# Optimization experiments

Measured on AMD Instinct MI355X. Metric: run time of the kernel, lower is better.

Reference implementation:

```python
import jax, jax.numpy as jnp
import numpy as np
import math

LENS = 64  # sliding window length (init arg `lens`)

def setup_inputs() -> dict:
    key = jax.random.key(0)
    k1, k2 = jax.random.split(key)
    N, D = 4096, 512
    X = jax.random.normal(k1, (N, D), dtype=jnp.float32)
    # nn.Linear(d, d, bias=False) weight, applied as x @ W.T
    W = jax.random.normal(k2, (D, D), dtype=jnp.float32) * (1.0 / math.sqrt(D))
    return {"X": X, "W": W}

def reference(X, W):
    N, d = X.shape
    B = N - LENS  # number of sliding windows
    # sliding-window gather: h_his[b] = X[b : b+LENS]
    idx = jnp.arange(B)[:, None] + jnp.arange(LENS)[None, :]  # [B, LENS]
    h_his = X[idx]            # [B, LENS, d]
    h_cur = X[LENS:]          # [B, d]  (index_cur = lens..N-1)
    # attention: score = bmm(linear(kv), q[..., None]) / sqrt(d)
    kv_proj = jnp.einsum('bld,ed->ble', h_his, W)            # [B, LENS, d]
    score = jnp.einsum('ble,be->bl', kv_proj, h_cur)[..., None] / math.sqrt(d)  # [B, LENS, 1]
    # faithful to original: softmax over last (size-1) axis -> all ones
    alpha = jax.nn.softmax(score, axis=-1)                   # [B, LENS, 1]
    attn_out = jnp.einsum('bl,bld->bd', alpha[..., 0], h_his)  # [B, d]
    # dropout(0.3) is eval-mode identity
    H = jnp.concatenate([X[:LENS], attn_out], axis=0) + X    # [N, d]
    h_cur_full = jnp.concatenate([X[:LENS], h_cur], axis=0)  # [N, d]
    return jnp.concatenate([H, h_cur_full], axis=-1)         # [N, 2d]
```

## Files before the change

kernel.cpp:

```cpp
#include <hip/hip_runtime.h>


#define LENS 64
#define RT 8
#define C4 128

__global__ __launch_bounds__(256) void chunk8_kernel(const float4* __restrict__ X4,
                                                     float4* __restrict__ C8,
                                                     int nChunks) {
    const int t  = blockIdx.x * 256 + threadIdx.x;
    const int c4 = t & (C4 - 1);
    const int k  = t >> 7;
    if (k >= nChunks) return;
    const float4* p = X4 + (size_t)k * 8 * C4 + c4;
    float4 s = make_float4(0.f, 0.f, 0.f, 0.f);
#pragma unroll
    for (int j = 0; j < 8; ++j) {
        float4 x = p[(size_t)j * C4];
        s.x += x.x; s.y += x.y; s.z += x.z; s.w += x.w;
    }
    C8[(size_t)k * C4 + c4] = s;
}

__global__ __launch_bounds__(256) void winsum_kernel(const float4* __restrict__ X4,
                                                     const float4* __restrict__ C8,
                                                     float4* __restrict__ O4,
                                                     int N) {
    const int c4   = threadIdx.x & (C4 - 1);
    const int half = threadIdx.x >> 7;
    const int i0   = blockIdx.x * (2 * RT) + half * RT;
    if (i0 >= N) return;

    if (i0 < LENS) {
#pragma unroll
        for (int k = 0; k < RT; ++k) {
            const int i = i0 + k;
            float4 x = X4[(size_t)i * C4 + c4];
            float4 h = make_float4(2.f * x.x, 2.f * x.y, 2.f * x.z, 2.f * x.w);
            O4[(size_t)i * (2 * C4) + c4]      = h;
            O4[(size_t)i * (2 * C4) + C4 + c4] = x;
        }
        return;
    }

    const int m = i0 >> 3;
    float4 w = make_float4(0.f, 0.f, 0.f, 0.f);
#pragma unroll
    for (int q = 0; q < 8; ++q) {
        float4 cs = C8[(size_t)(m - 8 + q) * C4 + c4];
        w.x += cs.x; w.y += cs.y; w.z += cs.z; w.w += cs.w;
    }

    float4 hist[RT - 1];
    const float4* ph = X4 + (size_t)(i0 - LENS) * C4 + c4;
#pragma unroll
    for (int j = 0; j < RT - 1; ++j) hist[j] = ph[(size_t)j * C4];

#pragma unroll
    for (int k = 0; k < RT; ++k) {
        const int i = i0 + k;
        float4 x = X4[(size_t)i * C4 + c4];
        float4 h = make_float4(x.x + w.x, x.y + w.y, x.z + w.z, x.w + w.w);
        O4[(size_t)i * (2 * C4) + c4]      = h;
        O4[(size_t)i * (2 * C4) + C4 + c4] = x;
        if (k < RT - 1) {
            float4 old = hist[k];
            w.x += x.x - old.x;
            w.y += x.y - old.y;
            w.z += x.z - old.z;
            w.w += x.w - old.w;
        }
    }
}

extern "C" void kernel_launch(void* const* d_in, const int* in_sizes, int n_in,
                              void* d_out, int out_size, void* d_ws, size_t ws_size,
                              hipStream_t stream) {
    const float* X = (const float*)d_in[0];
    float* O = (float*)d_out;
    float* C = (float*)d_ws;

    const int D = 512;
    const int N = in_sizes[0] / D;
    const int nChunks = N / 8;

    chunk8_kernel<<<(nChunks * C4 + 255) / 256, 256, 0, stream>>>(
        (const float4*)X, (float4*)C, nChunks);

    const int rows_per_block = 2 * RT;
    winsum_kernel<<<(N + rows_per_block - 1) / rows_per_block, 256, 0, stream>>>(
        (const float4*)X, (const float4*)C, (float4*)O, N);
}
```

Measured before the change: 69.30 us.

## Compute each output row independently instead of sliding running sum over rows

Replaces the per-thread sequential sliding-window update over 8 rows with one thread per output row element. Each thread sums 7 chunk partial sums plus 8 individual rows chosen by the row's offset within its chunk to form the window sum. This removes the serial dependency and raises parallelism 8x, at the cost of more loads per output (15 vs about 2 per row), mostly cache hits.

New measurement: 72.16 us. 1.04x slower.

```diff
diff --git a/kernel.cpp b/kernel.cpp
--- a/kernel.cpp
+++ b/kernel.cpp
@@ -2,7 +2,6 @@
 
 
 #define LENS 64
-#define RT 8
 #define C4 128
 
 __global__ __launch_bounds__(256) void chunk8_kernel(const float4* __restrict__ X4,
@@ -26,51 +25,39 @@
                                                      const float4* __restrict__ C8,
                                                      float4* __restrict__ O4,
                                                      int N) {
-    const int c4   = threadIdx.x & (C4 - 1);
-    const int half = threadIdx.x >> 7;
-    const int i0   = blockIdx.x * (2 * RT) + half * RT;
-    if (i0 >= N) return;
+    const int t  = blockIdx.x * 256 + threadIdx.x;
+    const int c4 = t & (C4 - 1);
+    const int i  = t >> 7;
+    if (i >= N) return;
 
-    if (i0 < LENS) {
-#pragma unroll
-        for (int k = 0; k < RT; ++k) {
-            const int i = i0 + k;
-            float4 x = X4[(size_t)i * C4 + c4];
-            float4 h = make_float4(2.f * x.x, 2.f * x.y, 2.f * x.z, 2.f * x.w);
-            O4[(size_t)i * (2 * C4) + c4]      = h;
-            O4[(size_t)i * (2 * C4) + C4 + c4] = x;
-        }
+    const float4 x = X4[(size_t)i * C4 + c4];
+
+    if (i < LENS) {
+        float4 h = make_float4(2.f * x.x, 2.f * x.y, 2.f * x.z, 2.f * x.w);
+        O4[(size_t)i * (2 * C4) + c4]      = h;
+        O4[(size_t)i * (2 * C4) + C4 + c4] = x;
         return;
     }
 
-    const int m = i0 >> 3;
+    const int p = i & 7;
+    const int k = (i >> 3) - 8;
+
     float4 w = make_float4(0.f, 0.f, 0.f, 0.f);
 #pragma unroll
-    for (int q = 0; q < 8; ++q) {
-        float4 cs = C8[(size_t)(m - 8 + q) * C4 + c4];
+    for (int q = 1; q <= 7; ++q) {
+        float4 cs = C8[(size_t)(k + q) * C4 + c4];
         w.x += cs.x; w.y += cs.y; w.z += cs.z; w.w += cs.w;
     }
+#pragma unroll
+    for (int j = 0; j < 8; ++j) {
+        const int r = 8 * k + j + ((j < p) ? 64 : 0);
+        float4 v = X4[(size_t)r * C4 + c4];
+        w.x += v.x; w.y += v.y; w.z += v.z; w.w += v.w;
+    }
 
-    float4 hist[RT - 1];
-    const float4* ph = X4 + (size_t)(i0 - LENS) * C4 + c4;
-#pragma unroll
-    for (int j = 0; j < RT - 1; ++j) hist[j] = ph[(size_t)j * C4];
-
-#pragma unroll
-    for (int k = 0; k < RT; ++k) {
-        const int i = i0 + k;
-        float4 x = X4[(size_t)i * C4 + c4];
-        float4 h = make_float4(x.x + w.x, x.y + w.y, x.z + w.z, x.w + w.w);
-        O4[(size_t)i * (2 * C4) + c4]      = h;
-        O4[(size_t)i * (2 * C4) + C4 + c4] = x;
-        if (k < RT - 1) {
-            float4 old = hist[k];
-            w.x += x.x - old.x;
-            w.y += x.y - old.y;
-            w.z += x.z - old.z;
-            w.w += x.w - old.w;
-        }
-    }
+    float4 h = make_float4(x.x + w.x, x.y + w.y, x.z + w.z, x.w + w.w);
+    O4[(size_t)i * (2 * C4) + c4]      = h;
+    O4[(size_t)i * (2 * C4) + C4 + c4] = x;
 }
 
 extern "C" void kernel_launch(void* const* d_in, const int* in_sizes, int n_in,
@@ -87,7 +74,6 @@
     chunk8_kernel<<<(nChunks * C4 + 255) / 256, 256, 0, stream>>>(
         (const float4*)X, (float4*)C, nChunks);
 
-    const int rows_per_block = 2 * RT;
-    winsum_kernel<<<(N + rows_per_block - 1) / rows_per_block, 256, 0, stream>>>(
+    winsum_kernel<<<(N * C4 + 255) / 256, 256, 0, stream>>>(
         (const float4*)X, (const float4*)C, (float4*)O, N);
 }
```
